# Kernel optimization log

Hardware: AMD Instinct MI355X
Metric: run time of the kernel (lower is better)

The kernel has to match this reference:

```python
import jax, jax.numpy as jnp
import numpy as np

DIM = 384
HEADS = 12
WH, WW = 7, 7
N = WH * WW
HEAD_DIM = DIM // HEADS
SCALE = HEAD_DIM ** -0.5


def _double_step_seq(step1, len1, step2, len2):
    seq1 = np.arange(0, step1 * len1, step1)
    seq2 = np.arange(0, step2 * len2, step2)
    return (seq1[:, None] + seq2[None, :]).reshape(1, -1)


def _rel_position_index():
    coords = _double_step_seq(2 * WW - 1, WH, 1, WW)  # (1, N)
    idx = coords + coords.T                            # (N, N)
    idx = idx[:, ::-1].copy()                          # flip along dim 1
    return jnp.asarray(idx, dtype=jnp.int32)

REL_IDX = _rel_position_index()


def setup_inputs() -> dict:
    key = jax.random.key(0)
    ks = jax.random.split(key, 6)
    B_ = 4096
    x = jax.random.normal(ks[0], (B_, N, DIM), dtype=jnp.float32)
    mask = jnp.zeros((64, N, N), dtype=jnp.float32)
    qkv_w = jax.random.normal(ks[1], (3 * DIM, DIM), dtype=jnp.float32) * 0.02
    qkv_b = jax.random.normal(ks[2], (3 * DIM,), dtype=jnp.float32) * 0.02
    proj_w = jax.random.normal(ks[3], (DIM, DIM), dtype=jnp.float32) * 0.02
    proj_b = jax.random.normal(ks[4], (DIM,), dtype=jnp.float32) * 0.02
    bias_table = jax.random.normal(ks[5], (169, HEADS), dtype=jnp.float32) * 0.02
    return {"x": x, "mask": mask, "qkv_w": qkv_w, "qkv_b": qkv_b,
            "proj_w": proj_w, "proj_b": proj_b, "bias_table": bias_table}


def reference(x, mask, qkv_w, qkv_b, proj_w, proj_b, bias_table):
    B_, n, C = x.shape
    # qkv projection: (B_, N, 3C) -> (3, B_, H, N, d)
    qkv = (x @ qkv_w.T + qkv_b).reshape(B_, n, 3, HEADS, HEAD_DIM)
    qkv = jnp.transpose(qkv, (2, 0, 3, 1, 4))
    q, k, v = qkv[0], qkv[1], qkv[2]
    q = q * SCALE
    attn = jnp.einsum('bhnd,bhmd->bhnm', q, k)  # (B_, H, N, N)
    # gathered relative position bias: (H, N, N)
    rel_bias = bias_table[REL_IDX.reshape(-1)].reshape(n, n, HEADS)
    rel_bias = jnp.transpose(rel_bias, (2, 0, 1))
    attn = attn + rel_bias[None]
    nW = mask.shape[0]
    attn = attn.reshape(B_ // nW, nW, HEADS, n, n) + mask[None, :, None]
    attn = attn.reshape(B_, HEADS, n, n)
    attn = jax.nn.softmax(attn, axis=-1)
    out = jnp.einsum('bhnm,bhmd->bnhd', attn, v).reshape(B_, n, C)
    out = out @ proj_w.T + proj_b
    return out
```

## Files before the change

### kernel.cpp

```cpp
#include <hip/hip_runtime.h>
#include <hip/hip_bf16.h>

#define NTOK 49
#define DIMC 384
#define NH 12
#define QSCALE 0.17677669529663687f

typedef __attribute__((ext_vector_type(8))) short short8;
typedef __attribute__((ext_vector_type(4))) float f32x4;
typedef unsigned int u32;

#define STG_OFF 0
#define KS_OFF  18432
#define VT_OFF  22528
#define PS_OFF  26624
#define QA_OFF  30720
#define BT_OFF  34816
#define QB_OFF  36848
#define SL_TOT  38000

#define NQFRAG (NH * 6 * 12)
#define WQB_SHORTS (NQFRAG * 512)
#define WPB_SHORTS (3 * 6 * 8192)
#define MB_TILES 1568
#define AV_BYTES ((size_t)MB_TILES * 6 * 16384)

__device__ __forceinline__ short f2bf(float f) {
    __bf16 h = (__bf16)f;
    return __builtin_bit_cast(short, h);
}
__device__ __forceinline__ float bf2f(short s) {
    u32 u = ((u32)(unsigned short)s) << 16;
    return __builtin_bit_cast(float, u);
}
__device__ __forceinline__ int cof(int p) { return 13 * (p / 7) + (p % 7); }

__device__ __forceinline__ void gld_lds16(const void* g, void* l) {
    __builtin_amdgcn_global_load_lds(
        (const __attribute__((address_space(1))) u32*)g,
        (__attribute__((address_space(3))) u32*)l, 16, 0, 0);
}

__device__ __forceinline__ short8 gather_bf(const float* __restrict__ w, int row, int k0) {
    const float* p = w + row * DIMC + k0;
    float4 a = *(const float4*)p;
    float4 b = *(const float4*)(p + 4);
    short8 r;
    r[0]=f2bf(a.x); r[1]=f2bf(a.y); r[2]=f2bf(a.z); r[3]=f2bf(a.w);
    r[4]=f2bf(b.x); r[5]=f2bf(b.y); r[6]=f2bf(b.z); r[7]=f2bf(b.w);
    return r;
}

__global__ void prep_weights(const float* __restrict__ qw, const float* __restrict__ pw,
                             short* __restrict__ wqb, short* __restrict__ wpb) {
    int gt = blockIdx.x * blockDim.x + threadIdx.x;
    if (gt < NQFRAG * 64) {
        int F = gt >> 6, lane = gt & 63;
        int h = F / 72, r = F % 72;
        int nt = r / 12, ks = r % 12;
        int l15 = lane & 15, l4 = lane >> 4;
        int grow = (nt >> 1) * DIMC + h * 32 + (nt & 1) * 16 + l15;
        const float* src = qw + grow * DIMC + ks * 32 + l4 * 8;
        short8 o;
        #pragma unroll
        for (int e = 0; e < 8; ++e) o[e] = f2bf(src[e]);
        *(short8*)(wqb + gt * 8) = o;
    } else if (gt < NQFRAG * 64 + 3 * 6 * 128 * 8) {
        int t2 = gt - NQFRAG * 64;
        int g  = t2 & 7;
        int r  = (t2 >> 3) & 127;
        int kc = (t2 >> 10) % 6;
        int nb = t2 / 6144;
        int k0 = kc * 64 + ((g ^ (r & 7)) << 3);
        const float* src = pw + (nb * 128 + r) * DIMC + k0;
        short8 o;
        #pragma unroll
        for (int e = 0; e < 8; ++e) o[e] = f2bf(src[e]);
        *(short8*)(wpb + (nb * 6 + kc) * 8192 + r * 64 + g * 8) = o;
    }
}

__global__ __launch_bounds__(256, 2)
void winattn_fused(const float* __restrict__ x, const float* __restrict__ mask,
                   const float* __restrict__ qkv_b, const float* __restrict__ bias_table,
                   const short* __restrict__ wqb, char* __restrict__ avb)
{
    __shared__ short SL[SL_TOT] __attribute__((aligned(128)));

    const int tid  = threadIdx.x;
    const int wv   = tid >> 6;
    const int lane = tid & 63;
    const int l15  = lane & 15;
    const int l4   = lane >> 4;
    const int win0 = blockIdx.x * 2;

    for (int i = tid; i < 169 * NH; i += 256) SL[BT_OFF + i] = f2bf(bias_table[i]);
    for (int i = tid; i < 3 * DIMC; i += 256) SL[QB_OFF + i] = f2bf(qkv_b[i]);

    short8 xf0[12], xf1[12];
    {
        const int row = wv * 16 + l15;
        const bool valid = row < NTOK;
        #pragma unroll
        for (int st = 0; st < 2; ++st) {
            const float* xr = x + (size_t)(win0 + st) * (NTOK * DIMC) + row * DIMC;
            #pragma unroll
            for (int ks = 0; ks < 12; ++ks) {
                short8 r;
                if (valid) {
                    float4 a = *(const float4*)(xr + ks * 32 + l4 * 8);
                    float4 b = *(const float4*)(xr + ks * 32 + l4 * 8 + 4);
                    r[0]=f2bf(a.x); r[1]=f2bf(a.y); r[2]=f2bf(a.z); r[3]=f2bf(a.w);
                    r[4]=f2bf(b.x); r[5]=f2bf(b.y); r[6]=f2bf(b.z); r[7]=f2bf(b.w);
                } else {
                    r = (short8)0;
                }
                if (st == 0) xf0[ks] = r; else xf1[ks] = r;
            }
        }
    }

    u32 mvp[2][4][2];
    int bidx[4][4];
    {
        #pragma unroll
        for (int st = 0; st < 2; ++st) {
            const float* maskp = mask + (size_t)((win0 + st) & 63) * (NTOK * NTOK);
            #pragma unroll
            for (int t = 0; t < 4; ++t) {
                int m = t * 16 + l15;
                float pad = (m < NTOK) ? 0.f : -1e30f;
                #pragma unroll
                for (int rp = 0; rp < 2; ++rp) {
                    float v[2];
                    #pragma unroll
                    for (int e = 0; e < 2; ++e) {
                        int i = wv * 16 + l4 * 4 + rp * 2 + e;
                        v[e] = ((i < NTOK && m < NTOK) ? maskp[i * NTOK + m] : 0.f) + pad;
                    }
                    mvp[st][t][rp] = (u32)(unsigned short)f2bf(v[0]) |
                                     ((u32)(unsigned short)f2bf(v[1]) << 16);
                }
            }
        }
        int cofi[4], cofm[4];
        #pragma unroll
        for (int t = 0; t < 4; ++t) {
            int m = t * 16 + l15;
            cofm[t] = cof(48 - (m < NTOK ? m : 48));
        }
        #pragma unroll
        for (int reg = 0; reg < 4; ++reg) {
            int i = wv * 16 + l4 * 4 + reg;
            cofi[reg] = cof(i < NTOK ? i : 48);
        }
        #pragma unroll
        for (int t = 0; t < 4; ++t)
            #pragma unroll
            for (int reg = 0; reg < 4; ++reg)
                bidx[t][reg] = (cofi[reg] + cofm[t]) * NH;
    }

    const f32x4 zf = (f32x4){0.f, 0.f, 0.f, 0.f};

    __syncthreads();

    #pragma unroll
    for (int pc = 0; pc < 2; ++pc) {
        #pragma unroll
        for (int t = 0; t < 3; ++t) {
            int jf = wv * 3 + t;
            int F = (jf >> 1) * 12 + 2 * pc + (jf & 1);
            gld_lds16(wqb + F * 512 + lane * 8, &SL[STG_OFF + pc * 6144 + jf * 512]);
        }
    }

    #pragma unroll 1
    for (int h = 0; h < NH; ++h) {
        f32x4 qa[12];
        #pragma unroll
        for (int t = 0; t < 12; ++t) qa[t] = zf;

        #pragma unroll
        for (int c = 0; c < 6; ++c) {
            asm volatile("s_waitcnt vmcnt(3)" ::: "memory");
            __builtin_amdgcn_s_barrier();
            __builtin_amdgcn_sched_barrier(0);
            {
                int cg2 = h * 6 + c + 2;
                if (cg2 >= 72) cg2 -= 72;
                int hh = cg2 / 6, cc = cg2 - hh * 6;
                #pragma unroll
                for (int t = 0; t < 3; ++t) {
                    int jf = wv * 3 + t;
                    int F = (hh * 6 + (jf >> 1)) * 12 + 2 * cc + (jf & 1);
                    gld_lds16(wqb + F * 512 + lane * 8,
                              &SL[STG_OFF + ((c + 2) % 3) * 6144 + jf * 512]);
                }
            }
            __builtin_amdgcn_sched_barrier(0);
            const short* buf = &SL[STG_OFF + (c % 3) * 6144];
            __builtin_amdgcn_s_setprio(1);
            #pragma unroll
            for (int j = 0; j < 12; ++j) {
                short8 b = *(const short8*)(buf + j * 512 + lane * 8);
                const int nt = j >> 1, kk = 2 * c + (j & 1);
                qa[nt]     = __builtin_amdgcn_mfma_f32_16x16x32_bf16(xf0[kk], b, qa[nt], 0, 0, 0);
                qa[6 + nt] = __builtin_amdgcn_mfma_f32_16x16x32_bf16(xf1[kk], b, qa[6 + nt], 0, 0, 0);
            }
            __builtin_amdgcn_s_setprio(0);
        }

        #pragma unroll
        for (int st = 0; st < 2; ++st) {
            #pragma unroll
            for (int nt = 0; nt < 6; ++nt) {
                const int sub = nt >> 1;
                const int colw = (nt & 1) * 16 + l15;
                const float bias = bf2f(SL[QB_OFF + sub * DIMC + h * 32 + colw]);
                #pragma unroll
                for (int reg = 0; reg < 4; ++reg) {
                    const int rl = l4 * 4 + reg;
                    const int tokg = wv * 16 + rl;
                    float val = qa[st * 6 + nt][reg] + bias;
                    if (sub == 0) {
                        int byt = rl * 64 + ((colw << 1) ^ ((rl & 3) << 4));
                        SL[QA_OFF + (wv * 2 + st) * 512 + (byt >> 1)] = f2bf(val * QSCALE);
                    } else if (sub == 1) {
                        int byt = tokg * 64 + ((colw << 1) ^ ((tokg & 3) << 4));
                        SL[KS_OFF + st * 2048 + (byt >> 1)] = f2bf(val);
                    } else {
                        int byt = colw * 128 + ((tokg << 1) ^ ((colw & 7) << 4));
                        SL[VT_OFF + st * 2048 + (byt >> 1)] = f2bf(val);
                    }
                }
            }
        }
        asm volatile("s_waitcnt lgkmcnt(0)" ::: "memory");
        __builtin_amdgcn_s_barrier();
        __builtin_amdgcn_sched_barrier(0);

        #pragma unroll
        for (int st = 0; st < 2; ++st) {
            short8 aq;
            {
                int byt = l15 * 64 + ((l4 * 16) ^ ((l15 & 3) << 4));
                aq = *(const short8*)&SL[QA_OFF + (wv * 2 + st) * 512 + (byt >> 1)];
            }
            f32x4 sc[4];
            #pragma unroll
            for (int t = 0; t < 4; ++t) {
                int row = t * 16 + l15;
                int byt = row * 64 + ((l4 * 16) ^ ((row & 3) << 4));
                short8 bk = *(const short8*)&SL[KS_OFF + st * 2048 + (byt >> 1)];
                sc[t] = __builtin_amdgcn_mfma_f32_16x16x32_bf16(aq, bk, zf, 0, 0, 0);
            }
            float p[4][4];
            #pragma unroll
            for (int t = 0; t < 4; ++t) {
                #pragma unroll
                for (int reg = 0; reg < 4; ++reg) {
                    u32 pk = mvp[st][t][reg >> 1];
                    float mval = bf2f((short)((reg & 1) ? (pk >> 16) : (pk & 0xffff)));
                    float bt = bf2f(SL[BT_OFF + bidx[t][reg] + h]);
                    p[t][reg] = sc[t][reg] + mval + bt;
                }
            }
            #pragma unroll
            for (int reg = 0; reg < 4; ++reg) {
                float mx = fmaxf(fmaxf(p[0][reg], p[1][reg]), fmaxf(p[2][reg], p[3][reg]));
                #pragma unroll
                for (int off = 8; off >= 1; off >>= 1) mx = fmaxf(mx, __shfl_xor(mx, off, 64));
                float s0 = 0.f;
                #pragma unroll
                for (int t = 0; t < 4; ++t) { p[t][reg] = __expf(p[t][reg] - mx); s0 += p[t][reg]; }
                #pragma unroll
                for (int off = 8; off >= 1; off >>= 1) s0 += __shfl_xor(s0, off, 64);
                float rs = 1.f / s0;
                #pragma unroll
                for (int t = 0; t < 4; ++t) p[t][reg] *= rs;
            }
            #pragma unroll
            for (int t = 0; t < 4; ++t)
                #pragma unroll
                for (int reg = 0; reg < 4; ++reg) {
                    int r = l4 * 4 + reg;
                    int byt = r * 128 + ((((t * 16 + l15) << 1)) ^ ((r & 7) << 4));
                    SL[PS_OFF + wv * 1024 + (byt >> 1)] = f2bf(p[t][reg]);
                }
            f32x4 av[2];
            av[0] = zf; av[1] = zf;
            #pragma unroll
            for (int kst = 0; kst < 2; ++kst) {
                short8 pa;
                {
                    int byt = l15 * 128 + (((kst * 64 + l4 * 16)) ^ ((l15 & 7) << 4));
                    pa = *(const short8*)&SL[PS_OFF + wv * 1024 + (byt >> 1)];
                }
                #pragma unroll
                for (int dt = 0; dt < 2; ++dt) {
                    int d = dt * 16 + l15;
                    int byt = d * 128 + (((kst * 64 + l4 * 16)) ^ ((d & 7) << 4));
                    short8 bv = *(const short8*)&SL[VT_OFF + st * 2048 + (byt >> 1)];
                    av[dt] = __builtin_amdgcn_mfma_f32_16x16x32_bf16(pa, bv, av[dt], 0, 0, 0);
                }
            }
            #pragma unroll
            for (int dt = 0; dt < 2; ++dt)
                #pragma unroll
                for (int reg = 0; reg < 4; ++reg) {
                    int tok = wv * 16 + l4 * 4 + reg;
                    if (tok < NTOK) {
                        int gt = (win0 + st) * NTOK + tok;
                        int mb = gt >> 7, r = gt & 127;
                        int inner = ((((h & 1) << 6) | ((dt * 16 + l15) << 1))) ^ ((r & 7) << 4);
                        *(short*)(avb + (size_t)(mb * 6 + (h >> 1)) * 16384 + r * 128 + inner)
                            = f2bf(av[dt][reg]);
                    }
                }
        }
    }
}

__global__ __launch_bounds__(256, 2)
void proj_gemm(const char* __restrict__ avb, const short* __restrict__ wpb,
               const float* __restrict__ proj_b, float* __restrict__ out)
{
    __shared__ char LC[2][32768] __attribute__((aligned(128)));

    const int tid = threadIdx.x;
    const int wv = tid >> 6, lane = tid & 63;
    const int l15 = lane & 15, l4 = lane >> 4;
    const int wr = wv >> 1, wc = wv & 1;
    const int mb = blockIdx.x / 3, nb = blockIdx.x % 3;

    const char* asrc = avb + (size_t)mb * 6 * 16384;
    const char* bsrc = (const char*)wpb + (size_t)nb * 6 * 16384;

    f32x4 acc[4][4];
    #pragma unroll
    for (int mi = 0; mi < 4; ++mi)
        #pragma unroll
        for (int ni = 0; ni < 4; ++ni) acc[mi][ni] = (f32x4){0.f, 0.f, 0.f, 0.f};

    #pragma unroll
    for (int it = 0; it < 4; ++it) {
        int L = (wv * 4 + it) * 1024;
        gld_lds16(asrc + L + lane * 16, &LC[0][L]);
        gld_lds16(bsrc + L + lane * 16, &LC[0][16384 + L]);
    }

    #pragma unroll
    for (int kc = 0; kc < 6; ++kc) {
        __builtin_amdgcn_sched_barrier(0);
        asm volatile("s_waitcnt vmcnt(0)" ::: "memory");
        __builtin_amdgcn_s_barrier();
        __builtin_amdgcn_sched_barrier(0);
        if (kc < 5) {
            #pragma unroll
            for (int it = 0; it < 4; ++it) {
                int L = (wv * 4 + it) * 1024;
                gld_lds16(asrc + (kc + 1) * 16384 + L + lane * 16, &LC[(kc + 1) & 1][L]);
                gld_lds16(bsrc + (kc + 1) * 16384 + L + lane * 16, &LC[(kc + 1) & 1][16384 + L]);
            }
        }
        const char* bufp = LC[kc & 1];
        __builtin_amdgcn_s_setprio(1);
        #pragma unroll
        for (int ksub = 0; ksub < 2; ++ksub) {
            short8 a[4], b[4];
            #pragma unroll
            for (int mi = 0; mi < 4; ++mi) {
                int row = wr * 64 + mi * 16 + l15;
                a[mi] = *(const short8*)(bufp + row * 128 +
                        ((ksub * 64 + l4 * 16) ^ ((row & 7) << 4)));
            }
            #pragma unroll
            for (int ni = 0; ni < 4; ++ni) {
                int row = wc * 64 + ni * 16 + l15;
                b[ni] = *(const short8*)(bufp + 16384 + row * 128 +
                        ((ksub * 64 + l4 * 16) ^ ((row & 7) << 4)));
            }
            #pragma unroll
            for (int mi = 0; mi < 4; ++mi)
                #pragma unroll
                for (int ni = 0; ni < 4; ++ni)
                    acc[mi][ni] = __builtin_amdgcn_mfma_f32_16x16x32_bf16(
                        a[mi], b[ni], acc[mi][ni], 0, 0, 0);
        }
        __builtin_amdgcn_s_setprio(0);
    }

    float pb[4];
    #pragma unroll
    for (int ni = 0; ni < 4; ++ni) pb[ni] = proj_b[nb * 128 + wc * 64 + ni * 16 + l15];
    #pragma unroll
    for (int mi = 0; mi < 4; ++mi) {
        #pragma unroll
        for (int ni = 0; ni < 4; ++ni) {
            #pragma unroll
            for (int reg = 0; reg < 4; ++reg) {
                size_t row = (size_t)(mb * 128 + wr * 64 + mi * 16 + l4 * 4 + reg);
                out[row * DIMC + nb * 128 + wc * 64 + ni * 16 + l15] = acc[mi][ni][reg] + pb[ni];
            }
        }
    }
}

__global__ __launch_bounds__(256, 2)
void winattn_fallback(const float* __restrict__ x, const float* __restrict__ mask,
                      const float* __restrict__ qkv_w, const float* __restrict__ qkv_b,
                      const float* __restrict__ proj_w, const float* __restrict__ proj_b,
                      const float* __restrict__ bias_table, float* __restrict__ out)
{
    __shared__ short SL[26624] __attribute__((aligned(128)));
    const int tid = threadIdx.x, wv = tid >> 6, lane = tid & 63;
    const int l15 = lane & 15, l4 = lane >> 4;
    const int win = blockIdx.x;
    const int xbase = win * (NTOK * DIMC);
    const int KSo = 0, VTo = 2048, PSo = 4096, QAo = 8192;

    short8 xf[12];
    {
        const int row = wv * 16 + l15;
        const bool valid = row < NTOK;
        const float* xr = x + xbase + row * DIMC;
        #pragma unroll
        for (int ks = 0; ks < 12; ++ks)
            xf[ks] = valid ? gather_bf(xr, 0, ks * 32 + l4 * 8) : (short8)0;
    }
    float mv[4][4]; int bidx[4][4]; float negm[4];
    {
        const float* maskp = mask + (win & 63) * (NTOK * NTOK);
        int cofi[4], cofm[4];
        #pragma unroll
        for (int t = 0; t < 4; ++t) {
            int m = t * 16 + l15;
            negm[t] = (m < NTOK) ? 0.f : -1e30f;
            cofm[t] = cof(48 - (m < NTOK ? m : 48));
            #pragma unroll
            for (int reg = 0; reg < 4; ++reg) {
                int i = wv * 16 + l4 * 4 + reg;
                mv[t][reg] = (i < NTOK && m < NTOK) ? maskp[i * NTOK + m] : 0.f;
            }
        }
        #pragma unroll
        for (int reg = 0; reg < 4; ++reg) {
            int i = wv * 16 + l4 * 4 + reg;
            cofi[reg] = cof(i < NTOK ? i : 48);
        }
        #pragma unroll
        for (int t = 0; t < 4; ++t)
            #pragma unroll
            for (int reg = 0; reg < 4; ++reg) bidx[t][reg] = (cofi[reg] + cofm[t]) * NH;
    }
    f32x4 pacc[24];
    #pragma unroll
    for (int t = 0; t < 24; ++t) pacc[t] = (f32x4){0.f, 0.f, 0.f, 0.f};
    const f32x4 zf = (f32x4){0.f, 0.f, 0.f, 0.f};
    __syncthreads();

    #pragma unroll 1
    for (int h = 0; h < NH; ++h) {
        f32x4 qa[6];
        #pragma unroll
        for (int nt = 0; nt < 6; ++nt) qa[nt] = zf;
        #pragma unroll
        for (int nt = 0; nt < 6; ++nt) {
            const int grow = (nt >> 1) * DIMC + h * 32 + (nt & 1) * 16 + l15;
            #pragma unroll
            for (int ks = 0; ks < 12; ++ks) {
                short8 b = gather_bf(qkv_w, grow, ks * 32 + l4 * 8);
                qa[nt] = __builtin_amdgcn_mfma_f32_16x16x32_bf16(xf[ks], b, qa[nt], 0, 0, 0);
            }
        }
        #pragma unroll
        for (int nt = 0; nt < 6; ++nt) {
            const int sub = nt >> 1;
            const int colw = (nt & 1) * 16 + l15;
            const float bias = qkv_b[sub * DIMC + h * 32 + colw];
            #pragma unroll
            for (int reg = 0; reg < 4; ++reg) {
                const int tokg = wv * 16 + l4 * 4 + reg;
                float val = qa[nt][reg] + bias;
                if (sub == 0) {
                    int byt = tokg * 64 + ((colw << 1) ^ ((tokg & 3) << 4));
                    SL[QAo + (byt >> 1)] = f2bf(val * QSCALE);
                } else if (sub == 1) {
                    int byt = tokg * 64 + ((colw << 1) ^ ((tokg & 3) << 4));
                    SL[KSo + (byt >> 1)] = f2bf(val);
                } else {
                    int byt = colw * 128 + ((tokg << 1) ^ ((colw & 7) << 4));
                    SL[VTo + (byt >> 1)] = f2bf(val);
                }
            }
        }
        __syncthreads();
        short8 aq;
        { int row = wv*16+l15; int byt = row*64 + ((l4*16) ^ ((row&3)<<4));
          aq = *(const short8*)&SL[QAo + (byt>>1)]; }
        f32x4 sc[4];
        #pragma unroll
        for (int t = 0; t < 4; ++t) {
            int row = t*16+l15; int byt = row*64 + ((l4*16) ^ ((row&3)<<4));
            short8 bk = *(const short8*)&SL[KSo + (byt>>1)];
            sc[t] = __builtin_amdgcn_mfma_f32_16x16x32_bf16(aq, bk, zf, 0, 0, 0);
        }
        float p[4][4];
        #pragma unroll
        for (int t = 0; t < 4; ++t)
            #pragma unroll
            for (int reg = 0; reg < 4; ++reg)
                p[t][reg] = sc[t][reg] + mv[t][reg] + bias_table[bidx[t][reg] + h] + negm[t];
        #pragma unroll
        for (int reg = 0; reg < 4; ++reg) {
            float mx = fmaxf(fmaxf(p[0][reg], p[1][reg]), fmaxf(p[2][reg], p[3][reg]));
            #pragma unroll
            for (int off = 8; off >= 1; off >>= 1) mx = fmaxf(mx, __shfl_xor(mx, off, 64));
            float s0 = 0.f;
            #pragma unroll
            for (int t = 0; t < 4; ++t) { p[t][reg] = __expf(p[t][reg] - mx); s0 += p[t][reg]; }
            #pragma unroll
            for (int off = 8; off >= 1; off >>= 1) s0 += __shfl_xor(s0, off, 64);
            float rs = 1.f / s0;
            #pragma unroll
            for (int t = 0; t < 4; ++t) p[t][reg] *= rs;
        }
        #pragma unroll
        for (int t = 0; t < 4; ++t)
            #pragma unroll
            for (int reg = 0; reg < 4; ++reg) {
                int row = wv*16 + l4*4 + reg;
                int byt = row*128 + (((t*16+l15) << 1) ^ ((row&7)<<4));
                SL[PSo + (byt>>1)] = f2bf(p[t][reg]);
            }
        f32x4 av[2]; av[0] = zf; av[1] = zf;
        #pragma unroll
        for (int kst = 0; kst < 2; ++kst) {
            short8 pa;
            { int row = wv*16+l15; int byt = row*128 + ((kst*64+l4*16) ^ ((row&7)<<4));
              pa = *(const short8*)&SL[PSo + (byt>>1)]; }
            #pragma unroll
            for (int dt = 0; dt < 2; ++dt) {
                int d = dt*16+l15; int byt = d*128 + ((kst*64+l4*16) ^ ((d&7)<<4));
                short8 bv = *(const short8*)&SL[VTo + (byt>>1)];
                av[dt] = __builtin_amdgcn_mfma_f32_16x16x32_bf16(pa, bv, av[dt], 0, 0, 0);
            }
        }
        __syncthreads();
        #pragma unroll
        for (int dt = 0; dt < 2; ++dt)
            #pragma unroll
            for (int reg = 0; reg < 4; ++reg) {
                int row = wv*16 + l4*4 + reg;
                int byt = row*64 + (((dt*16+l15) << 1) ^ ((row&3)<<4));
                SL[QAo + (byt>>1)] = f2bf(av[dt][reg]);
            }
        __syncthreads();
        short8 aa;
        { int row = wv*16+l15; int byt = row*64 + ((l4*16) ^ ((row&3)<<4));
          aa = *(const short8*)&SL[QAo + (byt>>1)]; }
        #pragma unroll
        for (int nt = 0; nt < 24; ++nt) {
            short8 bp = gather_bf(proj_w, nt * 16 + l15, h * 32 + l4 * 8);
            pacc[nt] = __builtin_amdgcn_mfma_f32_16x16x32_bf16(aa, bp, pacc[nt], 0, 0, 0);
        }
    }
    {
        float* op = out + xbase;
        #pragma unroll
        for (int nt = 0; nt < 24; ++nt) {
            const float pb = proj_b[nt * 16 + l15];
            #pragma unroll
            for (int reg = 0; reg < 4; ++reg) {
                const int i = wv * 16 + l4 * 4 + reg;
                if (i < NTOK) op[i * DIMC + nt * 16 + l15] = pacc[nt][reg] + pb;
            }
        }
    }
}

extern "C" void kernel_launch(void* const* d_in, const int* in_sizes, int n_in,
                              void* d_out, int out_size, void* d_ws, size_t ws_size,
                              hipStream_t stream) {
    const float* x          = (const float*)d_in[0];
    const float* mask       = (const float*)d_in[1];
    const float* qkv_w      = (const float*)d_in[2];
    const float* qkv_b      = (const float*)d_in[3];
    const float* proj_w     = (const float*)d_in[4];
    const float* proj_b     = (const float*)d_in[5];
    const float* bias_table = (const float*)d_in[6];
    float* out = (float*)d_out;

    const size_t need = (size_t)WQB_SHORTS * 2 + (size_t)WPB_SHORTS * 2 + AV_BYTES;
    if (ws_size >= need) {
        short* wqb = (short*)d_ws;
        short* wpb = wqb + WQB_SHORTS;
        char*  avb = (char*)(wpb + WPB_SHORTS);
        prep_weights<<<288, 256, 0, stream>>>(qkv_w, proj_w, wqb, wpb);
        winattn_fused<<<2048, 256, 0, stream>>>(x, mask, qkv_b, bias_table, wqb, avb);
        proj_gemm<<<MB_TILES * 3, 256, 0, stream>>>(avb, wpb, proj_b, out);
    } else {
        winattn_fallback<<<4096, 256, 0, stream>>>(x, mask, qkv_w, qkv_b, proj_w,
                                                   proj_b, bias_table, out);
    }
}
```

Measured before the change: 871.4 us.

## Process one window per block, load QKV weights directly, software-pipeline heads

Each block now handles a single window instead of two, which doubles the grid and halves the x-fragment registers. The LDS-staged, barrier-synchronized triple-buffered weight pipeline is replaced by direct global loads of weight fragments into registers, which shrinks LDS use. K/V are double-buffered by head parity so attention for head h-1 can interleave with the QKV projection for head h. The trade-off is that each block now re-reads the full QKV weight from global memory/L2 for only one window, doubling weight traffic, and weight-load latency is no longer hidden by the explicit LDS pipeline.

```diff
diff --git a/kernel.cpp b/kernel.cpp
--- a/kernel.cpp
+++ b/kernel.cpp
@@ -10,14 +10,13 @@
 typedef __attribute__((ext_vector_type(4))) float f32x4;
 typedef unsigned int u32;
 
-#define STG_OFF 0
-#define KS_OFF  18432
-#define VT_OFF  22528
-#define PS_OFF  26624
-#define QA_OFF  30720
-#define BT_OFF  34816
-#define QB_OFF  36848
-#define SL_TOT  38000
+#define KS_OFF  0
+#define VT_OFF  8192
+#define PS_OFF  12288
+#define QA_OFF  16384
+#define BT_OFF  18432
+#define QB_OFF  20464
+#define SL_TOT  21616
 
 #define NQFRAG (NH * 6 * 12)
 #define WQB_SHORTS (NQFRAG * 512)
@@ -92,55 +91,49 @@
     const int lane = tid & 63;
     const int l15  = lane & 15;
     const int l4   = lane >> 4;
-    const int win0 = blockIdx.x * 2;
+    const int win  = blockIdx.x;
 
     for (int i = tid; i < 169 * NH; i += 256) SL[BT_OFF + i] = f2bf(bias_table[i]);
     for (int i = tid; i < 3 * DIMC; i += 256) SL[QB_OFF + i] = f2bf(qkv_b[i]);
 
-    short8 xf0[12], xf1[12];
+    short8 xf[12];
     {
         const int row = wv * 16 + l15;
         const bool valid = row < NTOK;
-        #pragma unroll
-        for (int st = 0; st < 2; ++st) {
-            const float* xr = x + (size_t)(win0 + st) * (NTOK * DIMC) + row * DIMC;
-            #pragma unroll
-            for (int ks = 0; ks < 12; ++ks) {
-                short8 r;
-                if (valid) {
-                    float4 a = *(const float4*)(xr + ks * 32 + l4 * 8);
-                    float4 b = *(const float4*)(xr + ks * 32 + l4 * 8 + 4);
-                    r[0]=f2bf(a.x); r[1]=f2bf(a.y); r[2]=f2bf(a.z); r[3]=f2bf(a.w);
-                    r[4]=f2bf(b.x); r[5]=f2bf(b.y); r[6]=f2bf(b.z); r[7]=f2bf(b.w);
-                } else {
-                    r = (short8)0;
-                }
-                if (st == 0) xf0[ks] = r; else xf1[ks] = r;
-            }
-        }
-    }
-
-    u32 mvp[2][4][2];
+        const float* xr = x + (size_t)win * (NTOK * DIMC) + row * DIMC;
+        #pragma unroll
+        for (int ks = 0; ks < 12; ++ks) {
+            short8 r;
+            if (valid) {
+                float4 a = *(const float4*)(xr + ks * 32 + l4 * 8);
+                float4 b = *(const float4*)(xr + ks * 32 + l4 * 8 + 4);
+                r[0]=f2bf(a.x); r[1]=f2bf(a.y); r[2]=f2bf(a.z); r[3]=f2bf(a.w);
+                r[4]=f2bf(b.x); r[5]=f2bf(b.y); r[6]=f2bf(b.z); r[7]=f2bf(b.w);
+            } else {
+                r = (short8)0;
+            }
+            xf[ks] = r;
+        }
+    }
+
+    u32 mvp[4][2];
     int bidx[4][4];
     {
-        #pragma unroll
-        for (int st = 0; st < 2; ++st) {
-            const float* maskp = mask + (size_t)((win0 + st) & 63) * (NTOK * NTOK);
-            #pragma unroll
-            for (int t = 0; t < 4; ++t) {
-                int m = t * 16 + l15;
-                float pad = (m < NTOK) ? 0.f : -1e30f;
+        const float* maskp = mask + (size_t)(win & 63) * (NTOK * NTOK);
+        #pragma unroll
+        for (int t = 0; t < 4; ++t) {
+            int m = t * 16 + l15;
+            float pad = (m < NTOK) ? 0.f : -1e30f;
+            #pragma unroll
+            for (int rp = 0; rp < 2; ++rp) {
+                float v[2];
                 #pragma unroll
-                for (int rp = 0; rp < 2; ++rp) {
-                    float v[2];
-                    #pragma unroll
-                    for (int e = 0; e < 2; ++e) {
-                        int i = wv * 16 + l4 * 4 + rp * 2 + e;
-                        v[e] = ((i < NTOK && m < NTOK) ? maskp[i * NTOK + m] : 0.f) + pad;
-                    }
-                    mvp[st][t][rp] = (u32)(unsigned short)f2bf(v[0]) |
-                                     ((u32)(unsigned short)f2bf(v[1]) << 16);
+                for (int e = 0; e < 2; ++e) {
+                    int i = wv * 16 + l4 * 4 + rp * 2 + e;
+                    v[e] = ((i < NTOK && m < NTOK) ? maskp[i * NTOK + m] : 0.f) + pad;
                 }
+                mvp[t][rp] = (u32)(unsigned short)f2bf(v[0]) |
+                             ((u32)(unsigned short)f2bf(v[1]) << 16);
             }
         }
         int cofi[4], cofm[4];
@@ -165,161 +158,137 @@
 
     __syncthreads();
 
-    #pragma unroll
-    for (int pc = 0; pc < 2; ++pc) {
-        #pragma unroll
-        for (int t = 0; t < 3; ++t) {
-            int jf = wv * 3 + t;
-            int F = (jf >> 1) * 12 + 2 * pc + (jf & 1);
-            gld_lds16(wqb + F * 512 + lane * 8, &SL[STG_OFF + pc * 6144 + jf * 512]);
-        }
-    }
-
-    #pragma unroll 1
-    for (int h = 0; h < NH; ++h) {
-        f32x4 qa[12];
-        #pragma unroll
-        for (int t = 0; t < 12; ++t) qa[t] = zf;
-
+    auto qkv_head = [&](int h) {
+        const int p = h & 1;
+        f32x4 qa[6];
+        #pragma unroll
+        for (int nt = 0; nt < 6; ++nt) qa[nt] = zf;
+        const short* wq_h = wqb + (size_t)h * 36864 + lane * 8;
         #pragma unroll
         for (int c = 0; c < 6; ++c) {
-            asm volatile("s_waitcnt vmcnt(3)" ::: "memory");
-            __builtin_amdgcn_s_barrier();
-            __builtin_amdgcn_sched_barrier(0);
-            {
-                int cg2 = h * 6 + c + 2;
-                if (cg2 >= 72) cg2 -= 72;
-                int hh = cg2 / 6, cc = cg2 - hh * 6;
-                #pragma unroll
-                for (int t = 0; t < 3; ++t) {
-                    int jf = wv * 3 + t;
-                    int F = (hh * 6 + (jf >> 1)) * 12 + 2 * cc + (jf & 1);
-                    gld_lds16(wqb + F * 512 + lane * 8,
-                              &SL[STG_OFF + ((c + 2) % 3) * 6144 + jf * 512]);
-                }
-            }
-            __builtin_amdgcn_sched_barrier(0);
-            const short* buf = &SL[STG_OFF + (c % 3) * 6144];
-            __builtin_amdgcn_s_setprio(1);
-            #pragma unroll
-            for (int j = 0; j < 12; ++j) {
-                short8 b = *(const short8*)(buf + j * 512 + lane * 8);
-                const int nt = j >> 1, kk = 2 * c + (j & 1);
-                qa[nt]     = __builtin_amdgcn_mfma_f32_16x16x32_bf16(xf0[kk], b, qa[nt], 0, 0, 0);
-                qa[6 + nt] = __builtin_amdgcn_mfma_f32_16x16x32_bf16(xf1[kk], b, qa[6 + nt], 0, 0, 0);
-            }
-            __builtin_amdgcn_s_setprio(0);
-        }
-
-        #pragma unroll
-        for (int st = 0; st < 2; ++st) {
-            #pragma unroll
-            for (int nt = 0; nt < 6; ++nt) {
-                const int sub = nt >> 1;
-                const int colw = (nt & 1) * 16 + l15;
-                const float bias = bf2f(SL[QB_OFF + sub * DIMC + h * 32 + colw]);
-                #pragma unroll
-                for (int reg = 0; reg < 4; ++reg) {
-                    const int rl = l4 * 4 + reg;
-                    const int tokg = wv * 16 + rl;
-                    float val = qa[st * 6 + nt][reg] + bias;
-                    if (sub == 0) {
-                        int byt = rl * 64 + ((colw << 1) ^ ((rl & 3) << 4));
-                        SL[QA_OFF + (wv * 2 + st) * 512 + (byt >> 1)] = f2bf(val * QSCALE);
-                    } else if (sub == 1) {
-                        int byt = tokg * 64 + ((colw << 1) ^ ((tokg & 3) << 4));
-                        SL[KS_OFF + st * 2048 + (byt >> 1)] = f2bf(val);
-                    } else {
-                        int byt = colw * 128 + ((tokg << 1) ^ ((colw & 7) << 4));
-                        SL[VT_OFF + st * 2048 + (byt >> 1)] = f2bf(val);
-                    }
+            short8 bfr[12];
+            #pragma unroll
+            for (int j = 0; j < 12; ++j)
+                bfr[j] = *(const short8*)(wq_h + (((j >> 1) * 12) + 2 * c + (j & 1)) * 512);
+            #pragma unroll
+            for (int j = 0; j < 12; ++j)
+                qa[j >> 1] = __builtin_amdgcn_mfma_f32_16x16x32_bf16(
+                    xf[2 * c + (j & 1)], bfr[j], qa[j >> 1], 0, 0, 0);
+        }
+        #pragma unroll
+        for (int nt = 0; nt < 6; ++nt) {
+            const int sub = nt >> 1;
+            const int colw = (nt & 1) * 16 + l15;
+            const float bias = bf2f(SL[QB_OFF + sub * DIMC + h * 32 + colw]);
+            #pragma unroll
+            for (int reg = 0; reg < 4; ++reg) {
+                const int rl = l4 * 4 + reg;
+                const int tokg = wv * 16 + rl;
+                float val = qa[nt][reg] + bias;
+                if (sub == 0) {
+                    int byt = rl * 64 + ((colw << 1) ^ ((rl & 3) << 4));
+                    SL[QA_OFF + wv * 512 + (byt >> 1)] = f2bf(val * QSCALE);
+                } else if (sub == 1) {
+                    int byt = tokg * 128 + ((colw << 1) ^ ((tokg & 7) << 4));
+                    SL[KS_OFF + p * 4096 + (byt >> 1)] = f2bf(val);
+                } else {
+                    int byt = colw * 128 + ((tokg << 1) ^ ((colw & 7) << 4));
+                    SL[VT_OFF + p * 2048 + (byt >> 1)] = f2bf(val);
                 }
             }
         }
         asm volatile("s_waitcnt lgkmcnt(0)" ::: "memory");
         __builtin_amdgcn_s_barrier();
         __builtin_amdgcn_sched_barrier(0);
-
-        #pragma unroll
-        for (int st = 0; st < 2; ++st) {
-            short8 aq;
+    };
+
+    auto attn_head = [&](int hh) {
+        const int pp = hh & 1;
+        short8 aq;
+        {
+            int byt = l15 * 64 + ((l4 * 16) ^ ((l15 & 3) << 4));
+            aq = *(const short8*)&SL[QA_OFF + wv * 512 + (byt >> 1)];
+        }
+        f32x4 sc[4];
+        #pragma unroll
+        for (int t = 0; t < 4; ++t) {
+            int row = t * 16 + l15;
+            int byt = row * 128 + ((l4 * 16) ^ ((row & 7) << 4));
+            short8 bk = *(const short8*)&SL[KS_OFF + pp * 4096 + (byt >> 1)];
+            sc[t] = __builtin_amdgcn_mfma_f32_16x16x32_bf16(aq, bk, zf, 0, 0, 0);
+        }
+        float p[4][4];
+        #pragma unroll
+        for (int t = 0; t < 4; ++t) {
+            #pragma unroll
+            for (int reg = 0; reg < 4; ++reg) {
+                u32 pk = mvp[t][reg >> 1];
+                float mval = bf2f((short)((reg & 1) ? (pk >> 16) : (pk & 0xffff)));
+                float bt = bf2f(SL[BT_OFF + bidx[t][reg] + hh]);
+                p[t][reg] = sc[t][reg] + mval + bt;
+            }
+        }
+        #pragma unroll
+        for (int reg = 0; reg < 4; ++reg) {
+            float mx = fmaxf(fmaxf(p[0][reg], p[1][reg]), fmaxf(p[2][reg], p[3][reg]));
+            #pragma unroll
+            for (int off = 8; off >= 1; off >>= 1) mx = fmaxf(mx, __shfl_xor(mx, off, 64));
+            float s0 = 0.f;
+            #pragma unroll
+            for (int t = 0; t < 4; ++t) { p[t][reg] = __expf(p[t][reg] - mx); s0 += p[t][reg]; }
+            #pragma unroll
+            for (int off = 8; off >= 1; off >>= 1) s0 += __shfl_xor(s0, off, 64);
+            float rs = 1.f / s0;
+            #pragma unroll
+            for (int t = 0; t < 4; ++t) p[t][reg] *= rs;
+        }
+        #pragma unroll
+        for (int t = 0; t < 4; ++t)
+            #pragma unroll
+            for (int reg = 0; reg < 4; ++reg) {
+                int r = l4 * 4 + reg;
+                int byt = r * 128 + ((((t * 16 + l15) << 1)) ^ ((r & 7) << 4));
+                SL[PS_OFF + wv * 1024 + (byt >> 1)] = f2bf(p[t][reg]);
+            }
+        f32x4 av[2];
+        av[0] = zf; av[1] = zf;
+        #pragma unroll
+        for (int kst = 0; kst < 2; ++kst) {
+            short8 pa;
             {
-                int byt = l15 * 64 + ((l4 * 16) ^ ((l15 & 3) << 4));
-                aq = *(const short8*)&SL[QA_OFF + (wv * 2 + st) * 512 + (byt >> 1)];
-            }
-            f32x4 sc[4];
-            #pragma unroll
-            for (int t = 0; t < 4; ++t) {
-                int row = t * 16 + l15;
-                int byt = row * 64 + ((l4 * 16) ^ ((row & 3) << 4));
-                short8 bk = *(const short8*)&SL[KS_OFF + st * 2048 + (byt >> 1)];
-                sc[t] = __builtin_amdgcn_mfma_f32_16x16x32_bf16(aq, bk, zf, 0, 0, 0);
-            }
-            float p[4][4];
-            #pragma unroll
-            for (int t = 0; t < 4; ++t) {
-                #pragma unroll
-                for (int reg = 0; reg < 4; ++reg) {
-                    u32 pk = mvp[st][t][reg >> 1];
-                    float mval = bf2f((short)((reg & 1) ? (pk >> 16) : (pk & 0xffff)));
-                    float bt = bf2f(SL[BT_OFF + bidx[t][reg] + h]);
-                    p[t][reg] = sc[t][reg] + mval + bt;
+                int byt = l15 * 128 + (((kst * 64 + l4 * 16)) ^ ((l15 & 7) << 4));
+                pa = *(const short8*)&SL[PS_OFF + wv * 1024 + (byt >> 1)];
+            }
+            #pragma unroll
+            for (int dt = 0; dt < 2; ++dt) {
+                int d = dt * 16 + l15;
+                int byt = d * 128 + (((kst * 64 + l4 * 16)) ^ ((d & 7) << 4));
+                short8 bv = *(const short8*)&SL[VT_OFF + pp * 2048 + (byt >> 1)];
+                av[dt] = __builtin_amdgcn_mfma_f32_16x16x32_bf16(pa, bv, av[dt], 0, 0, 0);
+            }
+        }
+        #pragma unroll
+        for (int dt = 0; dt < 2; ++dt)
+            #pragma unroll
+            for (int reg = 0; reg < 4; ++reg) {
+                int tok = wv * 16 + l4 * 4 + reg;
+                if (tok < NTOK) {
+                    int gt = win * NTOK + tok;
+                    int mb = gt >> 7, r = gt & 127;
+                    int inner = ((((hh & 1) << 6) | ((dt * 16 + l15) << 1))) ^ ((r & 7) << 4);
+                    *(short*)(avb + (size_t)(mb * 6 + (hh >> 1)) * 16384 + r * 128 + inner)
+                        = f2bf(av[dt][reg]);
                 }
             }
-            #pragma unroll
-            for (int reg = 0; reg < 4; ++reg) {
-                float mx = fmaxf(fmaxf(p[0][reg], p[1][reg]), fmaxf(p[2][reg], p[3][reg]));
-                #pragma unroll
-                for (int off = 8; off >= 1; off >>= 1) mx = fmaxf(mx, __shfl_xor(mx, off, 64));
-                float s0 = 0.f;
-                #pragma unroll
-                for (int t = 0; t < 4; ++t) { p[t][reg] = __expf(p[t][reg] - mx); s0 += p[t][reg]; }
-                #pragma unroll
-                for (int off = 8; off >= 1; off >>= 1) s0 += __shfl_xor(s0, off, 64);
-                float rs = 1.f / s0;
-                #pragma unroll
-                for (int t = 0; t < 4; ++t) p[t][reg] *= rs;
-            }
-            #pragma unroll
-            for (int t = 0; t < 4; ++t)
-                #pragma unroll
-                for (int reg = 0; reg < 4; ++reg) {
-                    int r = l4 * 4 + reg;
-                    int byt = r * 128 + ((((t * 16 + l15) << 1)) ^ ((r & 7) << 4));
-                    SL[PS_OFF + wv * 1024 + (byt >> 1)] = f2bf(p[t][reg]);
-                }
-            f32x4 av[2];
-            av[0] = zf; av[1] = zf;
-            #pragma unroll
-            for (int kst = 0; kst < 2; ++kst) {
-                short8 pa;
-                {
-                    int byt = l15 * 128 + (((kst * 64 + l4 * 16)) ^ ((l15 & 7) << 4));
-                    pa = *(const short8*)&SL[PS_OFF + wv * 1024 + (byt >> 1)];
-                }
-                #pragma unroll
-                for (int dt = 0; dt < 2; ++dt) {
-                    int d = dt * 16 + l15;
-                    int byt = d * 128 + (((kst * 64 + l4 * 16)) ^ ((d & 7) << 4));
-                    short8 bv = *(const short8*)&SL[VT_OFF + st * 2048 + (byt >> 1)];
-                    av[dt] = __builtin_amdgcn_mfma_f32_16x16x32_bf16(pa, bv, av[dt], 0, 0, 0);
-                }
-            }
-            #pragma unroll
-            for (int dt = 0; dt < 2; ++dt)
-                #pragma unroll
-                for (int reg = 0; reg < 4; ++reg) {
-                    int tok = wv * 16 + l4 * 4 + reg;
-                    if (tok < NTOK) {
-                        int gt = (win0 + st) * NTOK + tok;
-                        int mb = gt >> 7, r = gt & 127;
-                        int inner = ((((h & 1) << 6) | ((dt * 16 + l15) << 1))) ^ ((r & 7) << 4);
-                        *(short*)(avb + (size_t)(mb * 6 + (h >> 1)) * 16384 + r * 128 + inner)
-                            = f2bf(av[dt][reg]);
-                    }
-                }
-        }
-    }
+    };
+
+    qkv_head(0);
+    #pragma unroll 1
+    for (int h = 1; h < NH; ++h) {
+        attn_head(h - 1);
+        qkv_head(h);
+    }
+    attn_head(NH - 1);
 }
 
 __global__ __launch_bounds__(256, 2)
@@ -598,7 +567,7 @@
         short* wpb = wqb + WQB_SHORTS;
         char*  avb = (char*)(wpb + WPB_SHORTS);
         prep_weights<<<288, 256, 0, stream>>>(qkv_w, proj_w, wqb, wpb);
-        winattn_fused<<<2048, 256, 0, stream>>>(x, mask, qkv_b, bias_table, wqb, avb);
+        winattn_fused<<<4096, 256, 0, stream>>>(x, mask, qkv_b, bias_table, wqb, avb);
         proj_gemm<<<MB_TILES * 3, 256, 0, stream>>>(avb, wpb, proj_b, out);
     } else {
         winattn_fallback<<<4096, 256, 0, stream>>>(x, mask, qkv_w, qkv_b, proj_w,
```

Measured after the change: 869.4 us. About the same (-0.2%).
